# Kernel tuning notes

Measured on AMD Instinct MI355X. Metric: run time of the kernel, lower is better.

The kernel has to match this reference:

```python
import jax, jax.numpy as jnp
import numpy as np

N = 50000          # nodes
E = 800000         # edges (before self-loops)
IN_CH = 16
HID = 32
HEADS = 4
NEG_SLOPE = 0.2    # PyG GATConv default leaky_relu slope


def add_self_loops(edge_index, n):
    loops = jnp.arange(n, dtype=edge_index.dtype)
    return jnp.concatenate([edge_index, jnp.stack([loops, loops])], axis=1)


def gat_layer(x, edge_index, W, a_src, a_dst, bias, heads, out_ch, concat):
    """PyG-style GATConv: gather -> attention logits -> segment softmax over dst -> scatter."""
    n = x.shape[0]
    h = (x @ W).reshape(n, heads, out_ch)            # [N, H, C]
    src, dst = edge_index[0], edge_index[1]          # messages flow src -> dst
    alpha_src = (h * a_src).sum(-1)                  # [N, H]
    alpha_dst = (h * a_dst).sum(-1)                  # [N, H]
    e = jax.nn.leaky_relu(alpha_src[src] + alpha_dst[dst], NEG_SLOPE)  # [Etot, H]
    # numerically stable segment softmax over incoming edges of each dst node
    e_max = jax.ops.segment_max(e, dst, num_segments=n)
    e_exp = jnp.exp(e - e_max[dst])
    denom = jax.ops.segment_sum(e_exp, dst, num_segments=n)
    alpha = e_exp / (denom[dst] + 1e-16)             # [Etot, H]
    out = jax.ops.segment_sum(h[src] * alpha[..., None], dst, num_segments=n)  # [N, H, C]
    out = out.reshape(n, heads * out_ch) if concat else out.mean(axis=1)
    return out + bias


def setup_inputs() -> dict:
    key = jax.random.key(0)
    ks = jax.random.split(key, 10)
    x = jax.random.normal(ks[0], (N, IN_CH), dtype=jnp.float32)
    edge_index = jax.random.randint(ks[1], (2, E), 0, N, dtype=jnp.int64)
    s = 0.1
    W1 = jax.random.normal(ks[2], (IN_CH, HEADS * HID), dtype=jnp.float32) * s
    a_src1 = jax.random.normal(ks[3], (1, HEADS, HID), dtype=jnp.float32) * s
    a_dst1 = jax.random.normal(ks[4], (1, HEADS, HID), dtype=jnp.float32) * s
    b1 = jnp.zeros((HEADS * HID,), dtype=jnp.float32)
    W2 = jax.random.normal(ks[5], (HEADS * HID, 2), dtype=jnp.float32) * s
    a_src2 = jax.random.normal(ks[6], (1, 1, 2), dtype=jnp.float32) * s
    a_dst2 = jax.random.normal(ks[7], (1, 1, 2), dtype=jnp.float32) * s
    b2 = jnp.zeros((2,), dtype=jnp.float32)
    return {"x": x, "edge_index": edge_index,
            "W1": W1, "a_src1": a_src1, "a_dst1": a_dst1, "b1": b1,
            "W2": W2, "a_src2": a_src2, "a_dst2": a_dst2, "b2": b2}


def reference(x, edge_index, W1, a_src1, a_dst1, b1, W2, a_src2, a_dst2, b2):
    ei = add_self_loops(edge_index, x.shape[0])
    h = gat_layer(x, ei, W1, a_src1, a_dst1, b1, HEADS, HID, concat=True)
    h = jax.nn.relu(h)
    out = gat_layer(h, ei, W2, a_src2, a_dst2, b2, 1, 2, concat=False)
    return out
```

## Files before the change

### kernel.cpp

```cpp
#include <hip/hip_runtime.h>
#include <hip/hip_bf16.h>

#define N_NODES 50000
#define N_EDGES 800000
#define ETOT    (N_EDGES + N_NODES)
#define STRIDE  64
#define IN_CH   16
#define HID     32
#define HEADS   4
#define C1      (HEADS * HID)
#define NEG     0.2f
#define NSLICE  8
#define SLICE_N (N_NODES / NSLICE)

#define DEG_BLOCKS  ((ETOT / 4 + 255) / 256)
#define FILL_BLOCKS (NSLICE * DEG_BLOCKS)
#define NGROUPS     (N_NODES / 4)
#define H1_BLOCKS   2048

typedef unsigned short u16;
typedef unsigned int   u32;

__device__ __forceinline__ float bf2f(u16 b) {
    return __uint_as_float(((u32)b) << 16);
}

__device__ __forceinline__ u16 f2bf(float f) {
    __hip_bfloat16 hb = __float2bfloat16(f);
    return *(u16*)&hb;
}

__device__ __forceinline__ int clampn(int v) {
    return v < 0 ? 0 : (v >= N_NODES ? N_NODES - 1 : v);
}

__device__ __forceinline__ int eidx(const int* ei, int e, int i64, int which) {
    int v = i64 ? ei[2 * (which * N_EDGES + e)] : ei[which * N_EDGES + e];
    return clampn(v);
}

__device__ __forceinline__ float cvt(const void* src, int i, int bf) {
    return bf ? bf2f(((const u16*)src)[i]) : ((const float*)src)[i];
}

__device__ __forceinline__ int probe_bf_wave(const u16* xb) {
    int l = threadIdx.x & 63;
    int my = 0;
#pragma unroll
    for (int k = 0; k < 4; k++) {
        float f = bf2f(xb[l * 4 + k]);
        float a = fabsf(f);
        if (f == 0.0f || (a > 9.5e-7f && a < 1.05e6f)) my++;
    }
#pragma unroll
    for (int m = 32; m; m >>= 1) my += __shfl_xor(my, m);
    return my >= 224;
}

__device__ __forceinline__ int probe_i64_wave(const int* ei32) {
    int l = threadIdx.x & 63;
    int nz = (l < 32 && ei32[2 * l + 1] != 0) ? 1 : 0;
#pragma unroll
    for (int m = 32; m; m >>= 1) nz += __shfl_xor(nz, m);
    return nz == 0;
}

__device__ __forceinline__ void dev_degfill(const int* __restrict__ ei,
                                            int* __restrict__ degs,
                                            u16* __restrict__ csr, int blk) {
    int slice = blk & (NSLICE - 1);
    int chunk = blk >> 3;
    int i64 = probe_i64_wave(ei);
    int e0 = (chunk * 256 + (int)threadIdx.x) * 4;
    if (e0 >= ETOT) return;
    int lo = slice * SLICE_N, hi = lo + SLICE_N;
    int s[4], d[4];
#pragma unroll
    for (int j = 0; j < 4; j++) {
        int e = e0 + j;
        if (e < N_EDGES) { s[j] = eidx(ei, e, i64, 0); d[j] = eidx(ei, e, i64, 1); }
        else             { s[j] = d[j] = e - N_EDGES; }
    }
#pragma unroll
    for (int j = 0; j < 4; j++) {
        if (d[j] >= lo && d[j] < hi) {
            u32 r = (u32)atomicAdd(&degs[d[j]], 1) + 1u;
            if (r < STRIDE) csr[(size_t)d[j] * STRIDE + r] = (u16)s[j];
        }
    }
}

__device__ __forceinline__ void dev_h1(const void* __restrict__ x,
                                       const void* __restrict__ W1,
                                       const void* __restrict__ a_s,
                                       const void* __restrict__ a_d,
                                       u32* __restrict__ h1u,
                                       float* __restrict__ as1,
                                       float* __restrict__ ad1, int blk) {
    int bf = probe_bf_wave((const u16*)x);
    if (blk == 0 && threadIdx.x < 4) as1[N_NODES * 4 + threadIdx.x] = -1e30f;
    if (blk == 0 && threadIdx.x >= 64 && threadIdx.x < 128)
        h1u[N_NODES * 64 + (threadIdx.x - 64)] = 0;

    int w = threadIdx.x >> 6, l = threadIdx.x & 63;

    float wa[IN_CH], wb[IN_CH];
    if (bf) {
        const u32* w32 = (const u32*)W1;
#pragma unroll
        for (int k = 0; k < IN_CH; k++) {
            u32 v = w32[k * 64 + l];
            wa[k] = bf2f((u16)(v & 0xFFFF));
            wb[k] = bf2f((u16)(v >> 16));
        }
    } else {
        const float2* w64 = (const float2*)W1;
#pragma unroll
        for (int k = 0; k < IN_CH; k++) {
            float2 v = w64[k * 64 + l];
            wa[k] = v.x; wb[k] = v.y;
        }
    }
    float asa, asb, ada, adb;
    if (bf) {
        u32 vs = ((const u32*)a_s)[l], vd = ((const u32*)a_d)[l];
        asa = bf2f((u16)(vs & 0xFFFF)); asb = bf2f((u16)(vs >> 16));
        ada = bf2f((u16)(vd & 0xFFFF)); adb = bf2f((u16)(vd >> 16));
    } else {
        float2 vs = ((const float2*)a_s)[l], vd = ((const float2*)a_d)[l];
        asa = vs.x; asb = vs.y; ada = vd.x; adb = vd.y;
    }

    for (int g = blk; g < NGROUPS; g += H1_BLOCKS) {
        int n = g * 4 + w;
        float xr[IN_CH];
        if (bf) {
            const uint4* xp = (const uint4*)((const u16*)x + (size_t)n * IN_CH);
            uint4 q0 = xp[0], q1 = xp[1];
            u32 qq[8] = {q0.x, q0.y, q0.z, q0.w, q1.x, q1.y, q1.z, q1.w};
#pragma unroll
            for (int k = 0; k < 8; k++) {
                xr[2 * k]     = bf2f((u16)(qq[k] & 0xFFFF));
                xr[2 * k + 1] = bf2f((u16)(qq[k] >> 16));
            }
        } else {
            const float4* xp = (const float4*)((const float*)x + (size_t)n * IN_CH);
#pragma unroll
            for (int k = 0; k < 4; k++) {
                float4 q = xp[k];
                xr[4 * k] = q.x; xr[4 * k + 1] = q.y;
                xr[4 * k + 2] = q.z; xr[4 * k + 3] = q.w;
            }
        }
        float acc0 = 0.f, acc1 = 0.f;
#pragma unroll
        for (int k = 0; k < IN_CH; k++) {
            acc0 += xr[k] * wa[k];
            acc1 += xr[k] * wb[k];
        }
        h1u[n * 64 + l] = (u32)f2bf(acc0) | ((u32)f2bf(acc1) << 16);

        float ps = acc0 * asa + acc1 * asb;
        float pd = acc0 * ada + acc1 * adb;
#pragma unroll
        for (int m = 8; m; m >>= 1) { ps += __shfl_xor(ps, m); pd += __shfl_xor(pd, m); }
        if ((l & 15) == 0) {
            int hd = l >> 4;
            as1[n * 4 + hd] = ps;
            ad1[n * 4 + hd] = pd;
        }
    }
}

__launch_bounds__(256)
__global__ void k_fill_h1(const void* __restrict__ x, const int* __restrict__ ei,
                          const void* __restrict__ W1, const void* __restrict__ a_s,
                          const void* __restrict__ a_d,
                          int* __restrict__ degs, u16* __restrict__ csr,
                          u32* __restrict__ h1u, float* __restrict__ as1,
                          float* __restrict__ ad1) {
    if (blockIdx.x < FILL_BLOCKS) { dev_degfill(ei, degs, csr, blockIdx.x); return; }
    dev_h1(x, W1, a_s, a_d, h1u, as1, ad1, blockIdx.x - FILL_BLOCKS);
}

__launch_bounds__(256)
__global__ void k_gather1(const void* __restrict__ x,
                          const int* __restrict__ degs, const u16* __restrict__ csr,
                          const u32* __restrict__ h1u,
                          const float* __restrict__ as1, const float* __restrict__ ad1,
                          const void* __restrict__ b1, const void* __restrict__ W2,
                          const void* __restrict__ a2s, const void* __restrict__ a2d,
                          float* __restrict__ h2, float* __restrict__ as2,
                          float* __restrict__ ad2) {
    int bf = probe_bf_wave((const u16*)x);
    int n = blockIdx.x * 4 + (threadIdx.x >> 6);
    int l = threadIdx.x & 63;
    int hd = l >> 4;
    int je = l & 7;
    int jh = (l >> 3) & 3;
    float advb = ad1[n * 4 + jh];
    int deg = degs[n] + 1;
    deg = deg > STRIDE ? STRIDE : deg;
    int nb = (deg + 7) >> 3;
    const u16* row = csr + (size_t)n * STRIDE;
    float acc0 = 0.f, acc1 = 0.f, swd = 0.f;

    int se = (int)row[je];
    if (se >= N_NODES) se = N_NODES;
    for (int b = 0; b < nb; b++) {
        int se_next = 0xFFFF;
        if (b + 1 < nb) se_next = (int)row[(b + 1) * 8 + je];
        float t = as1[se * 4 + jh] + advb;
        t = t > 0.f ? t : NEG * t;
        float wm = __expf(t);
        swd += wm;
#pragma unroll
        for (int j = 0; j < 8; j++) {
            int   sj = __shfl(se, j);
            float wj = __shfl(wm, hd * 8 + j);
            u32 p = h1u[sj * 64 + l];
            acc0 += wj * bf2f((u16)(p & 0xFFFF));
            acc1 += wj * bf2f((u16)(p >> 16));
        }
        se = se_next >= N_NODES ? N_NODES : se_next;
    }

    swd += __shfl_xor(swd, 1);
    swd += __shfl_xor(swd, 2);
    swd += __shfl_xor(swd, 4);
    float sw = __shfl(swd, hd * 8);

    float inv = 1.0f / sw;
    float v0 = acc0 * inv + cvt(b1, 2 * l, bf);
    float v1 = acc1 * inv + cvt(b1, 2 * l + 1, bf);
    v0 = v0 > 0.f ? v0 : 0.f;
    v1 = v1 > 0.f ? v1 : 0.f;
    float p0 = v0 * cvt(W2, 4 * l,     bf) + v1 * cvt(W2, 4 * l + 2, bf);
    float p1 = v0 * cvt(W2, 4 * l + 1, bf) + v1 * cvt(W2, 4 * l + 3, bf);
#pragma unroll
    for (int d = 32; d; d >>= 1) { p0 += __shfl_down(p0, d); p1 += __shfl_down(p1, d); }
    if (l == 0) {
        h2[n * 2] = p0; h2[n * 2 + 1] = p1;
        as2[n] = p0 * cvt(a2s, 0, bf) + p1 * cvt(a2s, 1, bf);
        ad2[n] = p0 * cvt(a2d, 0, bf) + p1 * cvt(a2d, 1, bf);
    }
}

__launch_bounds__(256)
__global__ void k_gather2(const void* __restrict__ x,
                          const int* __restrict__ degs, const u16* __restrict__ csr,
                          const float* __restrict__ h2, const float* __restrict__ as2,
                          const float* __restrict__ ad2, const void* __restrict__ b2,
                          void* __restrict__ out) {
    int bf = probe_bf_wave((const u16*)x);
    int n = blockIdx.x * 16 + (threadIdx.x >> 4);
    int g = threadIdx.x & 15;
    float adv = ad2[n], a0 = 0.f, a1 = 0.f, sw = 0.f;
    int deg = degs[n] + 1;
    deg = deg > STRIDE ? STRIDE : deg;
    const u16* row = csr + (size_t)n * STRIDE;
    for (int k = g; k < deg; k += 16) {
        int s = (int)row[k];
        float lg = as2[s] + adv;
        lg = lg > 0.f ? lg : NEG * lg;
        float w = __expf(lg);
        float2 hv = ((const float2*)h2)[s];
        a0 += w * hv.x;
        a1 += w * hv.y;
        sw += w;
    }
#pragma unroll
    for (int m = 8; m; m >>= 1) {
        a0 += __shfl_xor(a0, m); a1 += __shfl_xor(a1, m); sw += __shfl_xor(sw, m);
    }
    if (g == 0) {
        float inv = 1.0f / sw;
        float o0 = a0 * inv + cvt(b2, 0, bf);
        float o1 = a1 * inv + cvt(b2, 1, bf);
        if (bf) {
            ((u32*)out)[n] = (u32)f2bf(o0) | ((u32)f2bf(o1) << 16);
        } else {
            ((float2*)out)[n] = make_float2(o0, o1);
        }
    }
}

extern "C" void kernel_launch(void* const* d_in, const int* in_sizes, int n_in,
                              void* d_out, int out_size, void* d_ws, size_t ws_size,
                              hipStream_t stream) {
    const void* x    = d_in[0];
    const int*  ei   = (const int*)d_in[1];
    const void* W1   = d_in[2];
    const void* a_s1 = d_in[3];
    const void* a_d1 = d_in[4];
    const void* b1   = d_in[5];
    const void* W2   = d_in[6];
    const void* a_s2 = d_in[7];
    const void* a_d2 = d_in[8];
    const void* b2   = d_in[9];

    char* p = (char*)d_ws;
    int*   degs = (int*)p;     p += ((size_t)N_NODES * 4 + 255) & ~255;
    u16*   csr  = (u16*)p;     p += (size_t)N_NODES * STRIDE * 2;
    size_t init_bytes = (size_t)(p - (char*)d_ws);
    u32*   h1u  = (u32*)p;     p += (size_t)(N_NODES + 1) * 64 * 4;
    float* as1  = (float*)p;   p += (size_t)(N_NODES + 1) * HEADS * 4;
    float* ad1  = (float*)p;   p += (size_t)N_NODES * HEADS * 4;
    float* h2   = (float*)p;   p += (size_t)N_NODES * 2 * 4;
    float* as2  = (float*)p;   p += (size_t)N_NODES * 4;
    float* ad2  = (float*)p;   p += (size_t)N_NODES * 4;

    hipMemsetAsync(degs, 0xFF, init_bytes, stream);

    k_fill_h1<<<FILL_BLOCKS + H1_BLOCKS, 256, 0, stream>>>(
        x, ei, W1, a_s1, a_d1, degs, csr, h1u, as1, ad1);
    k_gather1<<<N_NODES / 4, 256, 0, stream>>>(
        x, degs, csr, h1u, as1, ad1, b1, W2, a_s2, a_d2, h2, as2, ad2);
    k_gather2<<<N_NODES / 16, 256, 0, stream>>>(
        x, degs, csr, h2, as2, ad2, b2, d_out);
}
```

Measured before the change: 199.0 us.

## Bucket edges by destination slice before CSR fill to avoid redundant edge reads

Replaces the old fill, where each of 8 slices re-read the whole edge list and kept only its own destinations, with a two-pass scheme. The first pass reads edges once, groups them by destination slice in shared memory and appends packed (src,dst-offset) words to per-slice global buckets. A second kernel then does the degree atomics and CSR writes for each slice. This adds a kernel launch, a memset and an extra global buffer round-trip, and it silently drops edges if a bucket overflows its fixed capacity. The old path is kept as a fallback when the workspace is too small.

```diff
diff --git a/kernel.cpp b/kernel.cpp
--- a/kernel.cpp
+++ b/kernel.cpp
@@ -12,9 +12,12 @@
 #define NEG     0.2f
 #define NSLICE  8
 #define SLICE_N (N_NODES / NSLICE)
+#define CAPB    112640
 
 #define DEG_BLOCKS  ((ETOT / 4 + 255) / 256)
-#define FILL_BLOCKS (NSLICE * DEG_BLOCKS)
+#define FILL2_PARTS 110
+#define FILL2_BLOCKS (NSLICE * FILL2_PARTS)
+#define FILLL_BLOCKS (NSLICE * DEG_BLOCKS)
 #define NGROUPS     (N_NODES / 4)
 #define H1_BLOCKS   2048
 
@@ -63,6 +66,88 @@
 #pragma unroll
     for (int m = 32; m; m >>= 1) nz += __shfl_xor(nz, m);
     return nz == 0;
+}
+
+__device__ __forceinline__ void dev_bucket(const int* __restrict__ ei,
+                                           u32* __restrict__ gcnt,
+                                           u32* __restrict__ gbuf,
+                                           u32* sbuf, u32* scnt, u32* sseg,
+                                           u32* sbase, int blk) {
+    int i64 = probe_i64_wave(ei);
+    if (threadIdx.x < NSLICE) scnt[threadIdx.x] = 0;
+    __syncthreads();
+    int e0 = (blk * 256 + (int)threadIdx.x) * 4;
+    int valid = (e0 < ETOT);
+    int bkt[4], pos[4]; u32 pk[4];
+    if (valid) {
+#pragma unroll
+        for (int j = 0; j < 4; j++) {
+            int e = e0 + j, s, d;
+            if (e < N_EDGES) { s = eidx(ei, e, i64, 0); d = eidx(ei, e, i64, 1); }
+            else             { s = d = e - N_EDGES; }
+            int b = d / SLICE_N;
+            bkt[j] = b;
+            pk[j]  = ((u32)s << 16) | (u32)(d - b * SLICE_N);
+            pos[j] = (int)atomicAdd(&scnt[b], 1u);
+        }
+    }
+    __syncthreads();
+    if (threadIdx.x == 0) {
+        u32 run = 0;
+        for (int b = 0; b < NSLICE; b++) { sseg[b] = run; run += scnt[b]; }
+    }
+    __syncthreads();
+    if (threadIdx.x < NSLICE)
+        sbase[threadIdx.x] = atomicAdd(&gcnt[threadIdx.x * 16], scnt[threadIdx.x]);
+    if (valid) {
+#pragma unroll
+        for (int j = 0; j < 4; j++) sbuf[sseg[bkt[j]] + pos[j]] = pk[j];
+    }
+    __syncthreads();
+#pragma unroll
+    for (int b = 0; b < NSLICE; b++) {
+        u32 cb = scnt[b], sb = sseg[b], gb = sbase[b];
+        for (u32 i = threadIdx.x; i < cb; i += 256) {
+            u32 o = gb + i;
+            if (o < CAPB) gbuf[(size_t)b * CAPB + o] = sbuf[sb + i];
+        }
+    }
+}
+
+__device__ __forceinline__ void dev_fill2(const u32* __restrict__ gcnt,
+                                          const u32* __restrict__ gbuf,
+                                          int* __restrict__ degs,
+                                          u16* __restrict__ csr, int blk) {
+    int s = blk & (NSLICE - 1);
+    int part = blk >> 3;
+    u32 cnt = gcnt[s * 16]; if (cnt > CAPB) cnt = CAPB;
+    u32 i0 = ((u32)part * 256 + (u32)threadIdx.x) * 4;
+    if (i0 >= cnt) return;
+    const u32* buf = gbuf + (size_t)s * CAPB;
+    u32 pk[4]; int nv;
+    if (i0 + 4 <= cnt) {
+        uint4 q = *(const uint4*)(buf + i0);
+        pk[0] = q.x; pk[1] = q.y; pk[2] = q.z; pk[3] = q.w; nv = 4;
+    } else {
+        nv = (int)(cnt - i0);
+#pragma unroll
+        for (int j = 0; j < 4; j++) if (j < nv) pk[j] = buf[i0 + j];
+    }
+    int base = s * SLICE_N;
+#pragma unroll
+    for (int j = 0; j < 4; j++) {
+        if (j < nv) {
+            int dst = base + (int)(pk[j] & 0xFFFFu);
+            u32 r = (u32)atomicAdd(&degs[dst], 1) + 1u;
+            if (r < STRIDE) csr[(size_t)dst * STRIDE + r] = (u16)(pk[j] >> 16);
+        }
+    }
+}
+
+__launch_bounds__(256)
+__global__ void k_fill2(const u32* __restrict__ gcnt, const u32* __restrict__ gbuf,
+                        int* __restrict__ degs, u16* __restrict__ csr) {
+    dev_fill2(gcnt, gbuf, degs, csr, blockIdx.x);
 }
 
 __device__ __forceinline__ void dev_degfill(const int* __restrict__ ei,
@@ -173,14 +258,30 @@
 }
 
 __launch_bounds__(256)
-__global__ void k_fill_h1(const void* __restrict__ x, const int* __restrict__ ei,
-                          const void* __restrict__ W1, const void* __restrict__ a_s,
-                          const void* __restrict__ a_d,
-                          int* __restrict__ degs, u16* __restrict__ csr,
-                          u32* __restrict__ h1u, float* __restrict__ as1,
-                          float* __restrict__ ad1) {
-    if (blockIdx.x < FILL_BLOCKS) { dev_degfill(ei, degs, csr, blockIdx.x); return; }
-    dev_h1(x, W1, a_s, a_d, h1u, as1, ad1, blockIdx.x - FILL_BLOCKS);
+__global__ void k_bucket_h1(const void* __restrict__ x, const int* __restrict__ ei,
+                            const void* __restrict__ W1, const void* __restrict__ a_s,
+                            const void* __restrict__ a_d,
+                            u32* __restrict__ gcnt, u32* __restrict__ gbuf,
+                            u32* __restrict__ h1u, float* __restrict__ as1,
+                            float* __restrict__ ad1) {
+    __shared__ u32 sbuf[1024];
+    __shared__ u32 scnt[NSLICE], sseg[NSLICE], sbase[NSLICE];
+    if (blockIdx.x < DEG_BLOCKS) {
+        dev_bucket(ei, gcnt, gbuf, sbuf, scnt, sseg, sbase, blockIdx.x);
+        return;
+    }
+    dev_h1(x, W1, a_s, a_d, h1u, as1, ad1, blockIdx.x - DEG_BLOCKS);
+}
+
+__launch_bounds__(256)
+__global__ void k_fill_h1_legacy(const void* __restrict__ x, const int* __restrict__ ei,
+                                 const void* __restrict__ W1, const void* __restrict__ a_s,
+                                 const void* __restrict__ a_d,
+                                 int* __restrict__ degs, u16* __restrict__ csr,
+                                 u32* __restrict__ h1u, float* __restrict__ as1,
+                                 float* __restrict__ ad1) {
+    if (blockIdx.x < FILLL_BLOCKS) { dev_degfill(ei, degs, csr, blockIdx.x); return; }
+    dev_h1(x, W1, a_s, a_d, h1u, as1, ad1, blockIdx.x - FILLL_BLOCKS);
 }
 
 __launch_bounds__(256)
@@ -303,17 +404,27 @@
     int*   degs = (int*)p;     p += ((size_t)N_NODES * 4 + 255) & ~255;
     u16*   csr  = (u16*)p;     p += (size_t)N_NODES * STRIDE * 2;
     size_t init_bytes = (size_t)(p - (char*)d_ws);
+    u32*   gcnt = (u32*)p;     p += 512;
     u32*   h1u  = (u32*)p;     p += (size_t)(N_NODES + 1) * 64 * 4;
     float* as1  = (float*)p;   p += (size_t)(N_NODES + 1) * HEADS * 4;
     float* ad1  = (float*)p;   p += (size_t)N_NODES * HEADS * 4;
     float* h2   = (float*)p;   p += (size_t)N_NODES * 2 * 4;
     float* as2  = (float*)p;   p += (size_t)N_NODES * 4;
     float* ad2  = (float*)p;   p += (size_t)N_NODES * 4;
+    u32*   gbuf = (u32*)p;     p += (size_t)NSLICE * CAPB * 4;
+    size_t need = (size_t)(p - (char*)d_ws);
 
     hipMemsetAsync(degs, 0xFF, init_bytes, stream);
 
-    k_fill_h1<<<FILL_BLOCKS + H1_BLOCKS, 256, 0, stream>>>(
-        x, ei, W1, a_s1, a_d1, degs, csr, h1u, as1, ad1);
+    if (ws_size >= need) {
+        hipMemsetAsync(gcnt, 0x00, 512, stream);
+        k_bucket_h1<<<DEG_BLOCKS + H1_BLOCKS, 256, 0, stream>>>(
+            x, ei, W1, a_s1, a_d1, gcnt, gbuf, h1u, as1, ad1);
+        k_fill2<<<FILL2_BLOCKS, 256, 0, stream>>>(gcnt, gbuf, degs, csr);
+    } else {
+        k_fill_h1_legacy<<<FILLL_BLOCKS + H1_BLOCKS, 256, 0, stream>>>(
+            x, ei, W1, a_s1, a_d1, degs, csr, h1u, as1, ad1);
+    }
     k_gather1<<<N_NODES / 4, 256, 0, stream>>>(
         x, degs, csr, h1u, as1, ad1, b1, W2, a_s2, a_d2, h2, as2, ad2);
     k_gather2<<<N_NODES / 16, 256, 0, stream>>>(
```

New measurement: 212.0 us. 1.07x slower.
